# Kernel optimization log

Hardware: AMD Instinct MI355X
Metric: run time of the kernel (lower is better)

Reference implementation:

```python
import jax, jax.numpy as jnp
import numpy as np

N = 15872   # number of predictions (31 * 512)
D = 129     # 128 image features + 1 objectness score
H = 128     # block MLP hidden width
IN = 2 * D + 1  # neighbor feats + main feats + add_info (IoU)
NUM_BLOCKS = 2


def _lin(k, fi, fo):
    return jax.random.normal(k, (fi, fo), jnp.float32) / np.sqrt(fi).astype(np.float32)


def setup_inputs() -> dict:
    key = jax.random.key(0)
    ks = jax.random.split(key, 24)
    # ragged neighborhood structure: mean size 16, exactly E = 16*N edges
    sizes = (np.arange(N) % 31) + 1
    E = int(sizes.sum())  # 253952
    rng = np.random.default_rng(0)
    nbr_idx = rng.integers(0, N, size=E).astype(np.int32)
    self_idx = np.repeat(np.arange(N, dtype=np.int32), sizes)  # sorted segment ids

    inp = {
        "interpolated": jax.random.normal(ks[0], (N, D), jnp.float32),
        "add_info": jax.random.uniform(ks[1], (E, 1), dtype=jnp.float32),
        "neighborhood_sizes": jnp.asarray(sizes, jnp.int32),
        "neighborhoods_indexes": jnp.asarray(nbr_idx),
        "self_indexes": jnp.asarray(self_idx),
    }
    # two (block, output) model pairs
    inp["b0_W1"] = _lin(ks[2], IN, H); inp["b0_b1"] = jnp.zeros((H,), jnp.float32)
    inp["b0_W2"] = _lin(ks[3], H, H);  inp["b0_b2"] = jnp.zeros((H,), jnp.float32)
    inp["b0_Wo"] = _lin(ks[4], H, D); inp["b0_bo"] = jnp.zeros((D,), jnp.float32)
    inp["b1_W1"] = _lin(ks[5], IN, H); inp["b1_b1"] = jnp.zeros((H,), jnp.float32)
    inp["b1_W2"] = _lin(ks[6], H, H);  inp["b1_b2"] = jnp.zeros((H,), jnp.float32)
    inp["b1_Wo"] = _lin(ks[7], H, D); inp["b1_bo"] = jnp.zeros((D,), jnp.float32)
    # final layers: 129 -> 64 -> 1
    inp["f_W1"] = _lin(ks[8], D, 64); inp["f_b1"] = jnp.zeros((64,), jnp.float32)
    inp["f_W2"] = _lin(ks[9], 64, 1); inp["f_b2"] = jnp.zeros((1,), jnp.float32)
    return inp


def _lnms_forward(interpolated, add_info, params, nbr_idx, self_idx):
    # params: list of (W1, b1, W2, b2, Wo, bo) per block, plus (fW1, fb1, fW2, fb2)
    for (W1, b1, W2, b2, Wo, bo) in params[:-1]:
        nbr = interpolated[nbr_idx]    # (E, D) gather of neighbor representations
        main = interpolated[self_idx]  # (E, D) gather of owning prediction
        x = jnp.concatenate([nbr, main, add_info], axis=1)  # (E, 2D+1)
        h = jax.nn.relu(x @ W1 + b1)
        h = jax.nn.relu(h @ W2 + b2)   # (E, H) processed neighborhoods
        # ragged per-neighborhood max pool (segments are contiguous/sorted)
        pooled = jax.ops.segment_max(h, self_idx, num_segments=N,
                                     indices_are_sorted=True)  # (N, H)
        block_output = pooled @ Wo + bo  # (N, D)
        interpolated = interpolated + block_output  # residual scatter-update
    fW1, fb1, fW2, fb2 = params[-1]
    return jax.nn.relu(interpolated @ fW1 + fb1) @ fW2 + fb2  # (N, 1)


def reference(interpolated, add_info,
              b0_W1, b0_b1, b0_W2, b0_b2, b0_Wo, b0_bo,
              b1_W1, b1_b1, b1_W2, b1_b2, b1_Wo, b1_bo,
              f_W1, f_b1, f_W2, f_b2,
              neighborhood_sizes, neighborhoods_indexes, self_indexes):
    params = [
        (b0_W1, b0_b1, b0_W2, b0_b2, b0_Wo, b0_bo),
        (b1_W1, b1_b1, b1_W2, b1_b2, b1_Wo, b1_bo),
        (f_W1, f_b1, f_W2, f_b2),
    ]
    return _lnms_forward(interpolated, add_info, params,
                         neighborhoods_indexes, self_indexes)
```

## Files before the change

### kernel.cpp

```cpp
#include <hip/hip_runtime.h>

#define NSEG 15872
#define DD 129
#define HH 128
#define NTILE (NSEG / 16)

typedef __attribute__((ext_vector_type(8))) short s16x8;
typedef __attribute__((ext_vector_type(4))) short s16x4;
typedef __attribute__((ext_vector_type(4))) float f32x4;
typedef __attribute__((ext_vector_type(16))) float f32x16;
typedef __attribute__((ext_vector_type(4))) unsigned u32x4;

__device__ __forceinline__ unsigned short f2bf(float x) {
  union { float f; unsigned u; } c; c.f = x;
  unsigned r = c.u + 0x7FFFu + ((c.u >> 16) & 1u);
  return (unsigned short)(r >> 16);
}
__device__ __forceinline__ float bf2f(unsigned short v) {
  union { unsigned u; float f; } c; c.u = ((unsigned)v) << 16; return c.f;
}

__global__ __launch_bounds__(1024) void scan_kernel(
    const int* __restrict__ sizes, int* __restrict__ offs) {
  extern __shared__ int dynS[];
  int* szS = dynS;
  int* tmpS = dynS + NSEG;
  __shared__ int sums[1024];
  const int t = threadIdx.x;

  for (int i = t; i < NSEG; i += 1024) szS[i] = sizes[i];
  __syncthreads();

  const int chunk = (NSEG + 1023) >> 10;
  const int s0 = t * chunk, s1 = min(s0 + chunk, NSEG);
  int s = 0;
  for (int i = s0; i < s1; ++i) s += szS[i];
  sums[t] = s;
  __syncthreads();
  for (int d = 1; d < 1024; d <<= 1) {
    int u = (t >= d) ? sums[t - d] : 0;
    __syncthreads();
    sums[t] += u;
    __syncthreads();
  }
  int a = sums[t] - s;
  for (int i = s0; i < s1; ++i) { tmpS[i] = a; a += szS[i]; }
  __syncthreads();
  for (int i = t; i < NSEG; i += 1024) offs[i] = tmpS[i];
  if (t == 1023) offs[NSEG] = a;
}

__device__ __forceinline__ void packB8(short* out, int idx8, const float* W,
                                       int N, int ld, int ncols, int kLimit,
                                       int rowBase) {
  const int n = (idx8 >> 3) % N;
  const int g = idx8 / (8 * N);
  s16x8 o;
#pragma unroll
  for (int i = 0; i < 8; ++i) {
    const int row = g * 8 + i;
    float v = 0.f;
    if (row < kLimit && n < ncols) v = W[(long)(rowBase + row) * ld + n];
    o[i] = (short)f2bf(v);
  }
  *(s16x8*)(out + idx8) = o;
}

__device__ __forceinline__ void packA1T8(short* out, int idx8, const float* W1) {
  const int unit = idx8 >> 3;
  const int lane = unit & 63;
  const int blk = unit >> 6;
  const int Mblk = blk / 10, ks = blk % 10;
  const int m = Mblk * 32 + (lane & 31);
  const int k0 = ks * 16 + ((lane >> 5) << 3);
  s16x8 o;
#pragma unroll
  for (int i = 0; i < 8; ++i) {
    const int k = k0 + i;
    o[i] = (short)((k < DD) ? f2bf(W1[(long)k * HH + m]) : 0);
  }
  *(s16x8*)(out + idx8) = o;
}

__device__ __forceinline__ void packB2T8(short* out, int idx8, const float* W2) {
  const int unit = idx8 >> 3;
  const int lane = unit & 63;
  const int blk = unit >> 6;
  const int ks = blk >> 2, nb = blk & 3;
  const int n = nb * 32 + (lane & 31);
  const int k0 = ks * 16 + ((lane >> 5) << 3);
  s16x8 o;
#pragma unroll
  for (int i = 0; i < 8; ++i)
    o[i] = (short)f2bf(W2[(long)(k0 + i) * HH + n]);
  *(s16x8*)(out + idx8) = o;
}

#define PACK_IDS 161792
#define TAB_IDS (NSEG * 160)
#define PACKV (PACK_IDS / 8)
#define TABV (TAB_IDS / 8)
#define PTBLK ((PACKV + TABV) / 256)
#define HMBLK (NTILE / 4)
__global__ __launch_bounds__(256) void pack_tab_kernel(
    const float* __restrict__ interp, unsigned short* __restrict__ tab,
    const float* __restrict__ W1b0, const float* __restrict__ W1b1,
    const float* __restrict__ W2b0, const float* __restrict__ W2b1,
    const float* __restrict__ Wob0, const float* __restrict__ Wob1,
    const float* __restrict__ fW1, short* __restrict__ PA1,
    short* __restrict__ PB2, short* __restrict__ PWo,
    short* __restrict__ PW1m, short* __restrict__ PfW1,
    const float* __restrict__ b1, float* __restrict__ Hm) {
  __shared__ short w1s[20480];
  const int bid = blockIdx.x;
  if (bid >= PTBLK) {
    const int hb = bid - PTBLK;
    for (int u = threadIdx.x; u < 2560; u += 256)
      packB8(w1s, u * 8, W1b0, 128, 128, 128, 129, 129);
    __syncthreads();
    const int lane = threadIdx.x & 63, w = threadIdx.x >> 6;
    const int lk = lane >> 4, n16 = lane & 15;
    const int tile = hb * 4 + w;
    const float* arow = interp + (long)(tile * 16 + n16) * DD;
    s16x8 A[5];
#pragma unroll
    for (int ks = 0; ks < 5; ++ks) {
      s16x8 o;
#pragma unroll
      for (int i = 0; i < 8; ++i) {
        const int k = ks * 32 + lk * 8 + i;
        o[i] = (short)((k < DD) ? f2bf(arow[k]) : 0);
      }
      A[ks] = o;
    }
    f32x4 C[8];
#pragma unroll
    for (int nf = 0; nf < 8; ++nf) C[nf] = (f32x4){0.f, 0.f, 0.f, 0.f};
#pragma unroll
    for (int ks = 0; ks < 5; ++ks)
#pragma unroll
      for (int nf = 0; nf < 8; ++nf) {
        const s16x8 b = *(const s16x8*)(w1s + (((ks * 4 + lk) * 128) + nf * 16 + n16) * 8);
        C[nf] = __builtin_amdgcn_mfma_f32_16x16x32_bf16(A[ks], b, C[nf], 0, 0, 0);
      }
#pragma unroll
    for (int nf = 0; nf < 8; ++nf) {
      const float bv = b1[nf * 16 + n16];
#pragma unroll
      for (int r = 0; r < 4; ++r)
        Hm[(long)(tile * 16 + lk * 4 + r) * HH + nf * 16 + n16] = C[nf][r] + bv;
    }
    return;
  }
  int vid = bid * 256 + threadIdx.x;
  if (vid < PACKV) {
    int idx = vid * 8;
    if (idx < 40960) {
      packA1T8(PA1 + (idx / 20480) * 20480, idx % 20480,
               (idx < 20480) ? W1b0 : W1b1);
      return;
    }
    idx -= 40960;
    if (idx < 32768) {
      packB2T8(PB2 + (idx / 16384) * 16384, idx % 16384,
               (idx < 16384) ? W2b0 : W2b1);
      return;
    }
    idx -= 32768;
    if (idx < 36864) {
      packB8(PWo + (idx / 18432) * 18432, idx % 18432,
             (idx < 18432) ? Wob0 : Wob1, 144, 129, 129, 128, 0);
      return;
    }
    idx -= 36864;
    if (idx < 40960) {
      packB8(PW1m + (idx / 20480) * 20480, idx % 20480,
             (idx < 20480) ? W1b0 : W1b1, 128, 128, 128, 129, 129);
      return;
    }
    idx -= 40960;
    packB8(PfW1, idx, fW1, 64, 64, 64, 129, 0);
    return;
  }
  vid -= PACKV;
  if (vid < TABV) {
    const int n = vid / 20;
    const int g = vid - n * 20;
    s16x8 o = (s16x8){0, 0, 0, 0, 0, 0, 0, 0};
    if (g < 16) {
      const float* src = interp + (long)n * DD + g * 8;
#pragma unroll
      for (int i = 0; i < 8; ++i) o[i] = (short)f2bf(src[i]);
    } else if (g == 16) {
      o[0] = (short)f2bf(interp[(long)n * DD + 128]);
    }
    *(s16x8*)(tab + (long)vid * 8) = o;
  }
}

__device__ __forceinline__ int pairEdge(int row, int oLo, int sLo, int oHi,
                                        int sHi) {
  int e = (row < sLo) ? (oLo + row) : (oHi + row - sLo);
  if (row >= sLo + sHi) e = oHi + sHi - 1;
  return e;
}

struct PairMeta {
  int segLo, segHi, oLo, sLo, oHi, sHi;
};

__device__ __forceinline__ void loadMeta(int p, PairMeta& M,
                                         const int* __restrict__ offs) {
  M.segLo = p;
  M.segHi = NSEG - 1 - p;
  M.oLo = offs[M.segLo]; M.sLo = offs[M.segLo + 1] - M.oLo;
  M.oHi = offs[M.segHi]; M.sHi = offs[M.segHi + 1] - M.oHi;
}

__device__ __forceinline__ void prefetchEdge(
    const PairMeta& M, int c, const int* __restrict__ nbrIdx,
    const float* __restrict__ iou, int n32, int& nbrow, float& io) {
  const int grow = (c << 5) + n32;
  const int e = pairEdge(grow, M.oLo, M.sLo, M.oHi, M.sHi);
  nbrow = nbrIdx[e];
  io = iou[e];
}

__device__ __forceinline__ void prefetchHm(
    const PairMeta& M, const float* __restrict__ Hm, int n32,
    float* hmLo, float* hmHi) {
#pragma unroll
  for (int q = 0; q < 4; ++q) {
    hmLo[q] = Hm[(long)M.segLo * HH + q * 32 + n32];
    hmHi[q] = Hm[(long)M.segHi * HH + q * 32 + n32];
  }
}

__device__ __forceinline__ void gatherX(const unsigned short* __restrict__ tab,
                                        int nbrow, int half, s16x8* X) {
  const unsigned short* ar = tab + (long)nbrow * 160;
#pragma unroll
  for (int ks = 0; ks < 9; ++ks)
    X[ks] = *(const s16x8*)(ar + ks * 16 + half * 8);
}

__device__ __forceinline__ void gemm1Phase(
    const PairMeta& M, int c, const s16x8* X, float io,
    const short* __restrict__ As1, const float* wvT,
    const float* hmLo, const float* hmHi,
    int lane, int half, int n32, s16x8* A2) {
  const int grow = (c << 5) + n32;
  const short oneBf = (short)0x3F80;
  s16x8 bb = (s16x8){0, 0, 0, 0, 0, 0, 0, 0};
  if (half == 0) {
    const bool lo = grow < M.sLo;
    bb[0] = lo ? oneBf : (short)0;
    bb[1] = bb[0];
    bb[2] = lo ? (short)0 : oneBf;
    bb[3] = bb[2];
    bb[4] = (short)f2bf(io);
  }
#pragma unroll
  for (int Mblk = 0; Mblk < 4; ++Mblk) {
    f32x16 C;
#pragma unroll
    for (int i = 0; i < 16; ++i) C[i] = 0.f;
#pragma unroll
    for (int ks = 0; ks < 9; ++ks) {
      const s16x8 a = *(const s16x8*)(As1 + ((Mblk * 10 + ks) * 64 + lane) * 8);
      C = __builtin_amdgcn_mfma_f32_32x32x16_bf16(a, X[ks], C, 0, 0, 0);
    }
    s16x8 ab = (s16x8){0, 0, 0, 0, 0, 0, 0, 0};
    if (half == 0) {
      const unsigned short p0 = f2bf(hmLo[Mblk]);
      ab[0] = (short)p0;
      ab[1] = (short)f2bf(hmLo[Mblk] - bf2f(p0));
      const unsigned short p1 = f2bf(hmHi[Mblk]);
      ab[2] = (short)p1;
      ab[3] = (short)f2bf(hmHi[Mblk] - bf2f(p1));
      ab[4] = (short)f2bf(wvT[Mblk]);
    }
    C = __builtin_amdgcn_mfma_f32_32x32x16_bf16(ab, bb, C, 0, 0, 0);
    unsigned wv[8];
#pragma unroll
    for (int j = 0; j < 8; ++j) {
      const float lo = fmaxf(C[2 * j], 0.f);
      const float hi = fmaxf(C[2 * j + 1], 0.f);
      asm("v_cvt_pk_bf16_f32 %0, %1, %2" : "=v"(wv[j]) : "v"(lo), "v"(hi));
    }
    asm("v_permlane32_swap_b32 %0, %1" : "+v"(wv[0]), "+v"(wv[2]));
    asm("v_permlane32_swap_b32 %0, %1" : "+v"(wv[1]), "+v"(wv[3]));
    asm("v_permlane32_swap_b32 %0, %1" : "+v"(wv[4]), "+v"(wv[6]));
    asm("v_permlane32_swap_b32 %0, %1" : "+v"(wv[5]), "+v"(wv[7]));
    union { u32x4 u; s16x8 s; } q0, q1;
    q0.u = (u32x4){wv[0], wv[1], wv[2], wv[3]};
    q1.u = (u32x4){wv[4], wv[5], wv[6], wv[7]};
    A2[2 * Mblk] = q0.s;
    A2[2 * Mblk + 1] = q1.s;
  }
}

__device__ __forceinline__ void gemm2Phase(
    const PairMeta& M, int c, const s16x8* A2, const short* __restrict__ Bs2,
    int lane, int half, int n32, float* mxLo, float* mxHi) {
#pragma unroll
  for (int nb = 0; nb < 4; ++nb) {
    f32x16 D;
#pragma unroll
    for (int i = 0; i < 16; ++i) D[i] = 0.f;
#pragma unroll
    for (int ks = 0; ks < 8; ++ks) {
      const s16x8 b = *(const s16x8*)(Bs2 + ((ks * 4 + nb) * 64 + lane) * 8);
      D = __builtin_amdgcn_mfma_f32_32x32x16_bf16(A2[ks], b, D, 0, 0, 0);
    }
#pragma unroll
    for (int reg = 0; reg < 16; ++reg) {
      const int rrow = (reg & 3) + 8 * (reg >> 2) + 4 * half;
      const int gr = (c << 5) + rrow;
      const float v = D[reg];
      if (gr < M.sLo) mxLo[nb] = fmaxf(mxLo[nb], v);
      else            mxHi[nb] = fmaxf(mxHi[nb], v);
    }
  }
}

__global__ __launch_bounds__(512, 2) void edge_kernel(
    const unsigned short* __restrict__ tab, const short* __restrict__ PA1,
    const short* __restrict__ PB2, const float* __restrict__ W1,
    const float* __restrict__ Hm, const float* __restrict__ iou,
    const int* __restrict__ nbrIdx, const int* __restrict__ offs,
    const float* __restrict__ b2, unsigned short* __restrict__ pooled) {
  extern __shared__ __align__(16) char smem[];
  short* As1 = (short*)smem;
  short* Bs2 = (short*)(smem + 40960);
  {
    const f32x4* s1 = (const f32x4*)PA1;
    f32x4* d1 = (f32x4*)As1;
    for (int i = threadIdx.x; i < 2560; i += 512) d1[i] = s1[i];
    const f32x4* s2 = (const f32x4*)PB2;
    f32x4* d2 = (f32x4*)Bs2;
    for (int i = threadIdx.x; i < 2048; i += 512) d2[i] = s2[i];
  }
  __syncthreads();

  const int lane = threadIdx.x & 63;
  const int w = __builtin_amdgcn_readfirstlane(threadIdx.x >> 6);
  const int half = lane >> 5, n32 = lane & 31;

  float b2v[4], wvT[4];
#pragma unroll
  for (int q = 0; q < 4; ++q) {
    b2v[q] = b2[q * 32 + n32];
    wvT[q] = W1[258 * HH + q * 32 + n32];
  }

  const int wid = (blockIdx.x << 3) + w;
  const int nw = gridDim.x << 3;
  const int npairs = NSEG >> 1;

  if (wid >= npairs) return;

  PairMeta M, Mn;
  int nbrow, nbrown;
  float io, ion;
  float hmLo[4], hmHi[4], hmLoN[4], hmHiN[4];
  loadMeta(wid, M, offs);
  prefetchEdge(M, 0, nbrIdx, iou, n32, nbrow, io);
  prefetchHm(M, Hm, n32, hmLo, hmHi);

  int p = wid;
  for (;;) {
    s16x8 X[9];
    gatherX(tab, nbrow, half, X);
    s16x8 A2[8];
    gemm1Phase(M, 0, X, io, As1, wvT, hmLo, hmHi, lane, half, n32, A2);
    const int pn = p + nw;
    const bool hn = pn < npairs;
    if (hn) {
      loadMeta(pn, Mn, offs);
      prefetchEdge(Mn, 0, nbrIdx, iou, n32, nbrown, ion);
      prefetchHm(Mn, Hm, n32, hmLoN, hmHiN);
    }
    float mxLo[4], mxHi[4];
#pragma unroll
    for (int q = 0; q < 4; ++q) { mxLo[q] = -3.4e38f; mxHi[q] = -3.4e38f; }
    gemm2Phase(M, 0, A2, Bs2, lane, half, n32, mxLo, mxHi);
    if (M.sLo + M.sHi > 32) {
      const int nchunk = (M.sLo + M.sHi + 31) >> 5;
      for (int c = 1; c < nchunk; ++c) {
        int nbf; float iof;
        prefetchEdge(M, c, nbrIdx, iou, n32, nbf, iof);
        gatherX(tab, nbf, half, X);
        gemm1Phase(M, c, X, iof, As1, wvT, hmLo, hmHi, lane, half, n32, A2);
        gemm2Phase(M, c, A2, Bs2, lane, half, n32, mxLo, mxHi);
      }
    }
#pragma unroll
    for (int nb = 0; nb < 4; ++nb) {
      float lo = fmaxf(mxLo[nb], __shfl_xor(mxLo[nb], 32, 64));
      float hi = fmaxf(mxHi[nb], __shfl_xor(mxHi[nb], 32, 64));
      if (half == 0) {
        pooled[(long)M.segLo * HH + nb * 32 + n32] = f2bf(fmaxf(lo + b2v[nb], 0.f));
        pooled[(long)M.segHi * HH + nb * 32 + n32] = f2bf(fmaxf(hi + b2v[nb], 0.f));
      }
    }
    if (!hn) break;
    M = Mn; nbrow = nbrown; io = ion;
#pragma unroll
    for (int q = 0; q < 4; ++q) { hmLo[q] = hmLoN[q]; hmHi[q] = hmHiN[q]; }
    p = pn;
  }
}

template <int NEXT>
__global__ __launch_bounds__(256) void resout_kernel(
    const unsigned short* __restrict__ pooled, const short* __restrict__ PWo,
    const float* __restrict__ bo, const float* __restrict__ resIn,
    float* __restrict__ resOut, unsigned short* __restrict__ tab,
    const short* __restrict__ PW1mN, const float* __restrict__ b1n,
    float* __restrict__ HmOut,
    const short* __restrict__ PfW1, const float* __restrict__ fb1,
    const float* __restrict__ fW2, const float* __restrict__ fb2,
    float* __restrict__ outFinal) {
  __shared__ short stS[4][16 * 168];
  const int lane = threadIdx.x & 63, w = threadIdx.x >> 6;
  const int lk = lane >> 4, n16 = lane & 15;
  short* st = stS[w];

  {
    const int row = lane >> 2, c0 = 129 + (lane & 3) * 8;
#pragma unroll
    for (int i = 0; i < 8; ++i) st[row * 168 + c0 + i] = 0;
  }

  const int tile = blockIdx.x * 4 + w;
  const unsigned short* arow = pooled + (long)(tile * 16 + n16) * HH;
  s16x8 A[4];
#pragma unroll
  for (int ks = 0; ks < 4; ++ks) A[ks] = *(const s16x8*)(arow + ks * 32 + lk * 8);
  f32x4 C[9];
#pragma unroll
  for (int nf = 0; nf < 9; ++nf) C[nf] = (f32x4){0.f, 0.f, 0.f, 0.f};
#pragma unroll
  for (int ks = 0; ks < 4; ++ks)
#pragma unroll
    for (int nf = 0; nf < 9; ++nf) {
      const s16x8 b = *(const s16x8*)(PWo + (((ks * 4 + lk) * 144) + nf * 16 + n16) * 8);
      C[nf] = __builtin_amdgcn_mfma_f32_16x16x32_bf16(A[ks], b, C[nf], 0, 0, 0);
    }

#pragma unroll
  for (int nf = 0; nf < 8; ++nf) {
    const int col = nf * 16 + n16;
    const float bov = bo[col];
#pragma unroll
    for (int r = 0; r < 4; ++r) {
      const int row = lk * 4 + r;
      const long node = tile * 16 + row;
      const float res = resIn[node * DD + col] + bov + C[nf][r];
      if (NEXT) {
        resOut[node * DD + col] = res;
        tab[node * 160 + col] = f2bf(res);
      }
      st[row * 168 + col] = (short)f2bf(res);
    }
  }
  if (n16 == 0) {
#pragma unroll
    for (int r = 0; r < 4; ++r) {
      const int row = lk * 4 + r;
      const long node = tile * 16 + row;
      const float res = resIn[node * DD + 128] + bo[128] + C[8][r];
      if (NEXT) {
        resOut[node * DD + 128] = res;
        tab[node * 160 + 128] = f2bf(res);
      }
      st[row * 168 + 128] = (short)f2bf(res);
    }
  }

  s16x8 A5[5];
#pragma unroll
  for (int ks = 0; ks < 5; ++ks)
    A5[ks] = *(const s16x8*)(st + n16 * 168 + ks * 32 + lk * 8);

  if (NEXT) {
    f32x4 H[8];
#pragma unroll
    for (int nf = 0; nf < 8; ++nf) H[nf] = (f32x4){0.f, 0.f, 0.f, 0.f};
#pragma unroll
    for (int ks = 0; ks < 5; ++ks)
#pragma unroll
      for (int nf = 0; nf < 8; ++nf) {
        const s16x8 b = *(const s16x8*)(PW1mN + (((ks * 4 + lk) * 128) + nf * 16 + n16) * 8);
        H[nf] = __builtin_amdgcn_mfma_f32_16x16x32_bf16(A5[ks], b, H[nf], 0, 0, 0);
      }
#pragma unroll
    for (int nf = 0; nf < 8; ++nf) {
      const float bv = b1n[nf * 16 + n16];
#pragma unroll
      for (int r = 0; r < 4; ++r)
        HmOut[(long)(tile * 16 + lk * 4 + r) * HH + nf * 16 + n16] = H[nf][r] + bv;
    }
  } else {
    f32x4 Ch[4];
#pragma unroll
    for (int nf = 0; nf < 4; ++nf) Ch[nf] = (f32x4){0.f, 0.f, 0.f, 0.f};
#pragma unroll
    for (int ks = 0; ks < 5; ++ks)
#pragma unroll
      for (int nf = 0; nf < 4; ++nf) {
        const s16x8 b = *(const s16x8*)(PfW1 + (((ks * 4 + lk) * 64) + nf * 16 + n16) * 8);
        Ch[nf] = __builtin_amdgcn_mfma_f32_16x16x32_bf16(A5[ks], b, Ch[nf], 0, 0, 0);
      }
    float b1v[4], w2v[4];
#pragma unroll
    for (int nf = 0; nf < 4; ++nf) {
      b1v[nf] = fb1[nf * 16 + n16];
      w2v[nf] = fW2[nf * 16 + n16];
    }
#pragma unroll
    for (int r = 0; r < 4; ++r) {
      float s = 0.f;
#pragma unroll
      for (int nf = 0; nf < 4; ++nf)
        s += fmaxf(Ch[nf][r] + b1v[nf], 0.f) * w2v[nf];
      s += __shfl_xor(s, 1, 64);
      s += __shfl_xor(s, 2, 64);
      s += __shfl_xor(s, 4, 64);
      s += __shfl_xor(s, 8, 64);
      if (n16 == 0) outFinal[tile * 16 + lk * 4 + r] = s + fb2[0];
    }
  }
}

extern "C" void kernel_launch(void* const* d_in, const int* in_sizes, int n_in,
                              void* d_out, int out_size, void* d_ws, size_t ws_size,
                              hipStream_t stream) {
  const float* interp  = (const float*)d_in[0];
  const float* addInfo = (const float*)d_in[1];
  const int* sizes     = (const int*)d_in[2];
  const int* nbrIdx    = (const int*)d_in[3];
  const float* b0W1 = (const float*)d_in[5];
  const float* b0b1 = (const float*)d_in[6];
  const float* b0W2 = (const float*)d_in[7];
  const float* b0b2 = (const float*)d_in[8];
  const float* b0Wo = (const float*)d_in[9];
  const float* b0bo = (const float*)d_in[10];
  const float* b1W1 = (const float*)d_in[11];
  const float* b1b1 = (const float*)d_in[12];
  const float* b1W2 = (const float*)d_in[13];
  const float* b1b2 = (const float*)d_in[14];
  const float* b1Wo = (const float*)d_in[15];
  const float* b1bo = (const float*)d_in[16];
  const float* fW1  = (const float*)d_in[17];
  const float* fb1  = (const float*)d_in[18];
  const float* fW2  = (const float*)d_in[19];
  const float* fb2  = (const float*)d_in[20];

  char* ws = (char*)d_ws;
  int*            offs  = (int*)(ws + 0);
  short*          PA1   = (short*)(ws + 65536);
  short*          PB2   = (short*)(ws + 147456);
  short*          PWo   = (short*)(ws + 212992);
  short*          PW1m  = (short*)(ws + 286720);
  short*          PfW1  = (short*)(ws + 368640);
  unsigned short* TAB   = (unsigned short*)(ws + 393216);
  float*          HM    = (float*)(ws + 5472256);
  unsigned short* POOLED= (unsigned short*)(ws + 13598720);
  float*          RES   = (float*)(ws + 17661952);

  scan_kernel<<<1, 1024, 2 * NSEG * sizeof(int), stream>>>(sizes, offs);
  pack_tab_kernel<<<PTBLK + HMBLK, 256, 0, stream>>>(
      interp, TAB, b0W1, b1W1, b0W2, b1W2, b0Wo, b1Wo, fW1,
      PA1, PB2, PWo, PW1m, PfW1, b0b1, HM);

  const size_t e_lds = 40960 + 32768;

  edge_kernel<<<496, 512, e_lds, stream>>>(TAB, PA1, PB2, b0W1, HM, addInfo,
                                           nbrIdx, offs, b0b2, POOLED);
  resout_kernel<1><<<NTILE / 4, 256, 0, stream>>>(
      POOLED, PWo, b0bo, interp, RES, TAB, PW1m + 20480, b1b1, HM,
      nullptr, nullptr, nullptr, nullptr, nullptr);

  edge_kernel<<<496, 512, e_lds, stream>>>(TAB, PA1 + 20480, PB2 + 16384, b1W1,
                                           HM, addInfo, nbrIdx, offs,
                                           b1b2, POOLED);
  resout_kernel<0><<<NTILE / 4, 256, 0, stream>>>(
      POOLED, PWo + 18432, b1bo, RES, nullptr, nullptr, nullptr, nullptr,
      nullptr, PfW1, fb1, fW2, fb2, (float*)d_out);
}
```

Baseline: 201.1 us.

## Fold offset scan into pack kernel and prefetch next pair's gather earlier

Removes the separate single-block scan launch by computing segment offsets in an extra block of the pack kernel, with a 256-thread scan reading sizes directly from global memory. In the edge kernel, the neighbor row gather for the next pair is now issued one iteration ahead, overlapping with the current GEMM2 (or after the chunk loop for large pairs), which keeps more registers live. The edge grid is halved to 248 blocks, giving each wave more pairs to loop over and more room to prefetch, at some cost in parallelism.

```diff
diff --git a/kernel.cpp b/kernel.cpp
--- a/kernel.cpp
+++ b/kernel.cpp
@@ -18,36 +18,6 @@
 }
 __device__ __forceinline__ float bf2f(unsigned short v) {
   union { unsigned u; float f; } c; c.u = ((unsigned)v) << 16; return c.f;
-}
-
-__global__ __launch_bounds__(1024) void scan_kernel(
-    const int* __restrict__ sizes, int* __restrict__ offs) {
-  extern __shared__ int dynS[];
-  int* szS = dynS;
-  int* tmpS = dynS + NSEG;
-  __shared__ int sums[1024];
-  const int t = threadIdx.x;
-
-  for (int i = t; i < NSEG; i += 1024) szS[i] = sizes[i];
-  __syncthreads();
-
-  const int chunk = (NSEG + 1023) >> 10;
-  const int s0 = t * chunk, s1 = min(s0 + chunk, NSEG);
-  int s = 0;
-  for (int i = s0; i < s1; ++i) s += szS[i];
-  sums[t] = s;
-  __syncthreads();
-  for (int d = 1; d < 1024; d <<= 1) {
-    int u = (t >= d) ? sums[t - d] : 0;
-    __syncthreads();
-    sums[t] += u;
-    __syncthreads();
-  }
-  int a = sums[t] - s;
-  for (int i = s0; i < s1; ++i) { tmpS[i] = a; a += szS[i]; }
-  __syncthreads();
-  for (int i = t; i < NSEG; i += 1024) offs[i] = tmpS[i];
-  if (t == 1023) offs[NSEG] = a;
 }
 
 __device__ __forceinline__ void packB8(short* out, int idx8, const float* W,
@@ -110,9 +80,35 @@
     const float* __restrict__ fW1, short* __restrict__ PA1,
     short* __restrict__ PB2, short* __restrict__ PWo,
     short* __restrict__ PW1m, short* __restrict__ PfW1,
-    const float* __restrict__ b1, float* __restrict__ Hm) {
+    const float* __restrict__ b1, float* __restrict__ Hm,
+    const int* __restrict__ sizes, int* __restrict__ offs) {
   __shared__ short w1s[20480];
   const int bid = blockIdx.x;
+  if (bid == PTBLK + HMBLK) {
+    int* sums = (int*)w1s;
+    const int t = threadIdx.x;
+    const int base = t * (NSEG / 256);
+    int s = 0;
+#pragma unroll 8
+    for (int i = 0; i < NSEG / 256; ++i) s += sizes[base + i];
+    sums[t] = s;
+    __syncthreads();
+    for (int d = 1; d < 256; d <<= 1) {
+      int u = (t >= d) ? sums[t - d] : 0;
+      __syncthreads();
+      sums[t] += u;
+      __syncthreads();
+    }
+    int a = sums[t] - s;
+#pragma unroll 8
+    for (int i = 0; i < NSEG / 256; ++i) {
+      const int sz = sizes[base + i];
+      offs[base + i] = a;
+      a += sz;
+    }
+    if (t == 255) offs[NSEG] = a;
+    return;
+  }
   if (bid >= PTBLK) {
     const int hb = bid - PTBLK;
     for (int u = threadIdx.x; u < 2560; u += 256)
@@ -361,31 +357,36 @@
   if (wid >= npairs) return;
 
   PairMeta M, Mn;
-  int nbrow, nbrown;
-  float io, ion;
+  float io, ioq;
   float hmLo[4], hmHi[4], hmLoN[4], hmHiN[4];
+  s16x8 X[9];
   loadMeta(wid, M, offs);
-  prefetchEdge(M, 0, nbrIdx, iou, n32, nbrow, io);
+  {
+    int nbq;
+    prefetchEdge(M, 0, nbrIdx, iou, n32, nbq, io);
+    gatherX(tab, nbq, half, X);
+  }
   prefetchHm(M, Hm, n32, hmLo, hmHi);
 
   int p = wid;
   for (;;) {
-    s16x8 X[9];
-    gatherX(tab, nbrow, half, X);
     s16x8 A2[8];
     gemm1Phase(M, 0, X, io, As1, wvT, hmLo, hmHi, lane, half, n32, A2);
     const int pn = p + nw;
     const bool hn = pn < npairs;
-    if (hn) {
+    const bool small = (M.sLo + M.sHi) <= 32;
+    if (small && hn) {
       loadMeta(pn, Mn, offs);
-      prefetchEdge(Mn, 0, nbrIdx, iou, n32, nbrown, ion);
+      int nbq;
+      prefetchEdge(Mn, 0, nbrIdx, iou, n32, nbq, ioq);
       prefetchHm(Mn, Hm, n32, hmLoN, hmHiN);
+      gatherX(tab, nbq, half, X);
     }
     float mxLo[4], mxHi[4];
 #pragma unroll
     for (int q = 0; q < 4; ++q) { mxLo[q] = -3.4e38f; mxHi[q] = -3.4e38f; }
     gemm2Phase(M, 0, A2, Bs2, lane, half, n32, mxLo, mxHi);
-    if (M.sLo + M.sHi > 32) {
+    if (!small) {
       const int nchunk = (M.sLo + M.sHi + 31) >> 5;
       for (int c = 1; c < nchunk; ++c) {
         int nbf; float iof;
@@ -394,6 +395,13 @@
         gemm1Phase(M, c, X, iof, As1, wvT, hmLo, hmHi, lane, half, n32, A2);
         gemm2Phase(M, c, A2, Bs2, lane, half, n32, mxLo, mxHi);
       }
+      if (hn) {
+        loadMeta(pn, Mn, offs);
+        int nbq;
+        prefetchEdge(Mn, 0, nbrIdx, iou, n32, nbq, ioq);
+        prefetchHm(Mn, Hm, n32, hmLoN, hmHiN);
+        gatherX(tab, nbq, half, X);
+      }
     }
 #pragma unroll
     for (int nb = 0; nb < 4; ++nb) {
@@ -405,7 +413,7 @@
       }
     }
     if (!hn) break;
-    M = Mn; nbrow = nbrown; io = ion;
+    M = Mn; io = ioq;
 #pragma unroll
     for (int q = 0; q < 4; ++q) { hmLo[q] = hmLoN[q]; hmHi[q] = hmHiN[q]; }
     p = pn;
@@ -570,20 +578,19 @@
   unsigned short* POOLED= (unsigned short*)(ws + 13598720);
   float*          RES   = (float*)(ws + 17661952);
 
-  scan_kernel<<<1, 1024, 2 * NSEG * sizeof(int), stream>>>(sizes, offs);
-  pack_tab_kernel<<<PTBLK + HMBLK, 256, 0, stream>>>(
+  pack_tab_kernel<<<PTBLK + HMBLK + 1, 256, 0, stream>>>(
       interp, TAB, b0W1, b1W1, b0W2, b1W2, b0Wo, b1Wo, fW1,
-      PA1, PB2, PWo, PW1m, PfW1, b0b1, HM);
+      PA1, PB2, PWo, PW1m, PfW1, b0b1, HM, sizes, offs);
 
   const size_t e_lds = 40960 + 32768;
 
-  edge_kernel<<<496, 512, e_lds, stream>>>(TAB, PA1, PB2, b0W1, HM, addInfo,
+  edge_kernel<<<248, 512, e_lds, stream>>>(TAB, PA1, PB2, b0W1, HM, addInfo,
                                            nbrIdx, offs, b0b2, POOLED);
   resout_kernel<1><<<NTILE / 4, 256, 0, stream>>>(
       POOLED, PWo, b0bo, interp, RES, TAB, PW1m + 20480, b1b1, HM,
       nullptr, nullptr, nullptr, nullptr, nullptr);
 
-  edge_kernel<<<496, 512, e_lds, stream>>>(TAB, PA1 + 20480, PB2 + 16384, b1W1,
+  edge_kernel<<<248, 512, e_lds, stream>>>(TAB, PA1 + 20480, PB2 + 16384, b1W1,
                                            HM, addInfo, nbrIdx, offs,
                                            b1b2, POOLED);
   resout_kernel<0><<<NTILE / 4, 256, 0, stream>>>(
```

New measurement: 180.3 us. 1.12x faster.
